# Kernel tuning notes

Measured on AMD Instinct MI355X. Metric: run time of the kernel, lower is better.

Reference implementation:

```python
import jax, jax.numpy as jnp
import numpy as np

N_NODES = 50000
N_EDGES = 400000
V = 3        # view_num
D = 128      # per-view input width (nfeat / view_num)
H = 128      # nhid


def setup_inputs() -> dict:
    key = jax.random.key(0)
    k_h, k_src, k_dst, k_w1, k_w2 = jax.random.split(key, 5)
    h = jax.random.normal(k_h, (N_NODES, V * D), dtype=jnp.float32)
    src = jax.random.randint(k_src, (N_EDGES,), 0, N_NODES, dtype=jnp.int32)
    dst = jax.random.randint(k_dst, (N_EDGES,), 0, N_NODES, dtype=jnp.int32)
    s1 = 1.0 / np.sqrt(D)
    s2 = 1.0 / np.sqrt(H)
    W1 = jax.random.uniform(k_w1, (V, D, H), dtype=jnp.float32, minval=-s1, maxval=s1)
    b1 = jnp.zeros((V, H), dtype=jnp.float32)
    W2 = jax.random.uniform(k_w2, (H, H), dtype=jnp.float32, minval=-s2, maxval=s2)
    b2 = jnp.zeros((H,), dtype=jnp.float32)
    return {"h": h, "src": src, "dst": dst, "W1": W1, "b1": b1, "W2": W2, "b2": b2}


def _agg(x, src, dst, n_nodes):
    # DGL GraphConv(norm='none') aggregation: out[d] = sum_{(s->d) in E} x[s]
    return jax.ops.segment_sum(x[src], dst, num_segments=n_nodes)


def reference(h, src, dst, W1, b1, W2, b2):
    n = h.shape[0]
    x = h.reshape(n, V, D)  # split into views along feature dim
    # layer 1 (per-view GraphConv + relu):  relu( A @ (x_v W1_v) + b1_v )
    xw = jnp.einsum('nvd,vdh->nvh', x, W1)
    y = jax.nn.relu(_agg(xw, src, dst, n) + b1)
    # dropout p=0 / eval mode -> identity
    # layer 2 (shared GraphConv + relu)
    yw = jnp.einsum('nvh,hk->nvk', y, W2)
    z = jax.nn.relu(_agg(yw, src, dst, n) + b2)
    # agg_type=0 -> plain concat of views
    return z.reshape(n, V * H)
```

## Files before the change

### kernel.cpp

```cpp
#include <hip/hip_runtime.h>

constexpr int NN = 50000;
constexpr int NE = 400000;
constexpr int NV = 3;
constexpr int DF = 128;
constexpr int F  = 384;
constexpr int TR = 32;
constexpr int NB = (NN + 255) / 256;
constexpr int SP = 136;

typedef short  bf16x8 __attribute__((ext_vector_type(8)));
typedef float  f32x4  __attribute__((ext_vector_type(4)));


__device__ __forceinline__ ushort f2bf(float f) {
  unsigned u = __float_as_uint(f);
  u = (u + 0x7fffu + ((u >> 16) & 1u)) >> 16;
  return (ushort)u;
}


__device__ __forceinline__ void wprep_one(const float* __restrict__ W,
                                          ushort* __restrict__ pk, int idx) {
  int j = idx & 7, lane = (idx >> 3) & 63, cb = (idx >> 9) & 7, kb = (idx >> 12) & 3;
  int vs = idx >> 14;
  int v = vs >> 1, s = vs & 1;
  int d = kb * 32 + (lane >> 4) * 8 + j;
  int c = cb * 16 + (lane & 15);
  float w = W[((size_t)v * DF + d) * DF + c];
  ushort hi = f2bf(w);
  ushort outv = hi;
  if (s) outv = f2bf(w - __uint_as_float((unsigned)hi << 16));
  pk[idx] = outv;
}

constexpr int WB1 = (NV * 2 * 16384) / 256;
constexpr int WB2 = (2 * 16384) / 256;

__global__ void k_prep0(const float* __restrict__ W1, const float* __restrict__ W2,
                        ushort* __restrict__ w1pk, ushort* __restrict__ w2pk,
                        int* __restrict__ deg) {
  int b = blockIdx.x, t = threadIdx.x;
  if (b < WB1) {
    wprep_one(W1, w1pk, b * 256 + t);
  } else if (b < WB1 + WB2) {
    wprep_one(W2, w2pk, (b - WB1) * 256 + t);
  } else {
    int i = (b - WB1 - WB2) * 256 + t;
    if (i < NN) deg[i] = 0;
  }
}


__global__ void k_cvtcnt(const float* __restrict__ in, ushort* __restrict__ outb,
                         const int* __restrict__ dst, int* __restrict__ deg) {
  int b = blockIdx.x, t = threadIdx.x;
  if (b < 2048) {
    const int n4 = NN * F / 4;
    const float4* in4 = (const float4*)in;
    for (int k = b * 256 + t; k < n4; k += 2048 * 256) {
      float4 x = in4[k];
      ushort4 u;
      u.x = f2bf(x.x); u.y = f2bf(x.y); u.z = f2bf(x.z); u.w = f2bf(x.w);
      *(ushort4*)(outb + (size_t)k * 4) = u;
    }
  } else {
    for (int e = (b - 2048) * 256 + t; e < NE; e += 1024 * 256)
      atomicAdd(&deg[dst[e]], 1);
  }
}


__global__ void k_blocksum(const int* __restrict__ deg, int* __restrict__ bsum) {
  __shared__ int s[4];
  int i = blockIdx.x * 256 + threadIdx.x;
  int v = (i < NN) ? deg[i] : 0;
  for (int o = 32; o > 0; o >>= 1) v += __shfl_down(v, o);
  if ((threadIdx.x & 63) == 0) s[threadIdx.x >> 6] = v;
  __syncthreads();
  if (threadIdx.x == 0) bsum[blockIdx.x] = s[0] + s[1] + s[2] + s[3];
}

__global__ void k_scanpar(int* __restrict__ bsum, int* __restrict__ offs_n) {
  __shared__ int s[256];
  int t = threadIdx.x;
  int v = (t < NB) ? bsum[t] : 0;
  s[t] = v;
  __syncthreads();
  for (int o = 1; o < 256; o <<= 1) {
    int add = (t >= o) ? s[t - o] : 0;
    __syncthreads();
    s[t] += add;
    __syncthreads();
  }
  if (t < NB) bsum[t] = s[t] - v;
  if (t == NB - 1) *offs_n = s[t];
}

__global__ void k_offsets(const int* __restrict__ deg, const int* __restrict__ bsum,
                          int* __restrict__ offs) {
  __shared__ int s[256];
  int t = threadIdx.x;
  int i = blockIdx.x * 256 + t;
  int v = (i < NN) ? deg[i] : 0;
  s[t] = v;
  __syncthreads();
  for (int o = 1; o < 256; o <<= 1) {
    int add = (t >= o) ? s[t - o] : 0;
    __syncthreads();
    s[t] += add;
    __syncthreads();
  }
  if (i < NN) offs[i] = bsum[blockIdx.x] + s[t] - v;
}

__global__ void k_scatter(const int* __restrict__ src, const int* __restrict__ dst,
                          const int* __restrict__ offs, int* __restrict__ deg,
                          int* __restrict__ csr) {
  int i = blockIdx.x * blockDim.x + threadIdx.x;
  int stride = gridDim.x * blockDim.x;
  for (int e = i; e < NE; e += stride) {
    int d = dst[e];
    int pos = offs[d] + atomicSub(&deg[d], 1) - 1;
    csr[pos] = src[e];
  }
}


template <bool OUT_BF16>
__global__ __launch_bounds__(256, 4)
void k_layer(const ushort* __restrict__ feat,
             const int* __restrict__ offs, const int* __restrict__ csr,
             const ushort* __restrict__ Wpk, int vmul,
             const float* __restrict__ ball, int bstride,
             void* __restrict__ outp) {
  __shared__ ushort sThi[TR][SP];
  __shared__ ushort sTlo[TR][SP];
  const int t = threadIdx.x;
  const int v = blockIdx.y;
  const float* __restrict__ bias = ball + (size_t)v * bstride;

  const int wave = t >> 6, lane = t & 63;
  const int lane15 = lane & 15, lgrp = lane >> 4;
  const int row0 = blockIdx.x * TR;
  const int vcol = v * DF + lane * 2;
  const int lane2 = lane * 2;

  const int base = row0 + wave * 8;

  int ow = 0;
  {
    int ri = base + lane;
    if (lane <= 8) {
      if (ri > NN) ri = NN;
      ow = offs[ri];
    }
  }
  int so[9];
#pragma unroll
  for (int k = 0; k < 9; ++k) so[k] = __builtin_amdgcn_readlane(ow, k);

  float ax[8], ay[8];
#pragma unroll
  for (int r = 0; r < 8; ++r) { ax[r] = 0.f; ay[r] = 0.f; }

  const int eb = so[0], ee = so[8];
  for (int chunk = eb; chunk < ee; chunk += 64) {
    int ce = chunk + lane; if (ce > ee - 1) ce = ee - 1;
    int idx = csr[ce];
    int cend = chunk + 64 < ee ? chunk + 64 : ee;
#pragma unroll
    for (int r = 0; r < 8; ++r) {
      int js = so[r] > chunk ? so[r] : chunk;
      int je = so[r + 1] < cend ? so[r + 1] : cend;
      int j  = js - chunk;
      int jn = je - chunk;
      for (; j + 4 <= jn; j += 4) {
        int s0 = __builtin_amdgcn_readlane(idx, j);
        int s1 = __builtin_amdgcn_readlane(idx, j + 1);
        int s2 = __builtin_amdgcn_readlane(idx, j + 2);
        int s3 = __builtin_amdgcn_readlane(idx, j + 3);
        unsigned u0 = *(const unsigned*)(feat + (size_t)s0 * F + vcol);
        unsigned u1 = *(const unsigned*)(feat + (size_t)s1 * F + vcol);
        unsigned u2 = *(const unsigned*)(feat + (size_t)s2 * F + vcol);
        unsigned u3 = *(const unsigned*)(feat + (size_t)s3 * F + vcol);
        ax[r] += __uint_as_float(u0 << 16); ay[r] += __uint_as_float(u0 & 0xffff0000u);
        ax[r] += __uint_as_float(u1 << 16); ay[r] += __uint_as_float(u1 & 0xffff0000u);
        ax[r] += __uint_as_float(u2 << 16); ay[r] += __uint_as_float(u2 & 0xffff0000u);
        ax[r] += __uint_as_float(u3 << 16); ay[r] += __uint_as_float(u3 & 0xffff0000u);
      }
      for (; j < jn; ++j) {
        int s0 = __builtin_amdgcn_readlane(idx, j);
        unsigned u0 = *(const unsigned*)(feat + (size_t)s0 * F + vcol);
        ax[r] += __uint_as_float(u0 << 16); ay[r] += __uint_as_float(u0 & 0xffff0000u);
      }
    }
  }

#pragma unroll
  for (int r = 0; r < 8; ++r) {
    ushort hx = f2bf(ax[r]);
    ushort lx = f2bf(ax[r] - __uint_as_float((unsigned)hx << 16));
    ushort hy = f2bf(ay[r]);
    ushort ly = f2bf(ay[r] - __uint_as_float((unsigned)hy << 16));
    *(unsigned*)&sThi[wave * 8 + r][lane2] = (unsigned)hx | ((unsigned)hy << 16);
    *(unsigned*)&sTlo[wave * 8 + r][lane2] = (unsigned)lx | ((unsigned)ly << 16);
  }
  __syncthreads();

  const ushort* pkbase = Wpk + (size_t)(v * vmul) * (2 * 4 * 8 * 512);
  const float bv0 = bias[wave * 32 + lane15];
  const float bv1 = bias[wave * 32 + 16 + lane15];
  f32x4 acc00 = {bv0, bv0, bv0, bv0};
  f32x4 acc01 = {bv1, bv1, bv1, bv1};
  f32x4 acc10 = {bv0, bv0, bv0, bv0};
  f32x4 acc11 = {bv1, bv1, bv1, bv1};

#pragma unroll
  for (int kb = 0; kb < 4; ++kb) {
    const int acol = kb * 32 + lgrp * 8;
    bf16x8 ah0 = *(const bf16x8*)&sThi[lane15][acol];
    bf16x8 ah1 = *(const bf16x8*)&sThi[16 + lane15][acol];
    bf16x8 al0 = *(const bf16x8*)&sTlo[lane15][acol];
    bf16x8 al1 = *(const bf16x8*)&sTlo[16 + lane15][acol];
    bf16x8 bh0 = *(const bf16x8*)(pkbase + ((size_t)((0 * 4 + kb) * 8 + wave * 2 + 0)) * 512 + lane * 8);
    bf16x8 bh1 = *(const bf16x8*)(pkbase + ((size_t)((0 * 4 + kb) * 8 + wave * 2 + 1)) * 512 + lane * 8);
    bf16x8 bl0 = *(const bf16x8*)(pkbase + ((size_t)((1 * 4 + kb) * 8 + wave * 2 + 0)) * 512 + lane * 8);
    bf16x8 bl1 = *(const bf16x8*)(pkbase + ((size_t)((1 * 4 + kb) * 8 + wave * 2 + 1)) * 512 + lane * 8);
    acc00 = __builtin_amdgcn_mfma_f32_16x16x32_bf16(ah0, bh0, acc00, 0, 0, 0);
    acc00 = __builtin_amdgcn_mfma_f32_16x16x32_bf16(al0, bh0, acc00, 0, 0, 0);
    acc00 = __builtin_amdgcn_mfma_f32_16x16x32_bf16(ah0, bl0, acc00, 0, 0, 0);
    acc01 = __builtin_amdgcn_mfma_f32_16x16x32_bf16(ah0, bh1, acc01, 0, 0, 0);
    acc01 = __builtin_amdgcn_mfma_f32_16x16x32_bf16(al0, bh1, acc01, 0, 0, 0);
    acc01 = __builtin_amdgcn_mfma_f32_16x16x32_bf16(ah0, bl1, acc01, 0, 0, 0);
    acc10 = __builtin_amdgcn_mfma_f32_16x16x32_bf16(ah1, bh0, acc10, 0, 0, 0);
    acc10 = __builtin_amdgcn_mfma_f32_16x16x32_bf16(al1, bh0, acc10, 0, 0, 0);
    acc10 = __builtin_amdgcn_mfma_f32_16x16x32_bf16(ah1, bl0, acc10, 0, 0, 0);
    acc11 = __builtin_amdgcn_mfma_f32_16x16x32_bf16(ah1, bh1, acc11, 0, 0, 0);
    acc11 = __builtin_amdgcn_mfma_f32_16x16x32_bf16(al1, bh1, acc11, 0, 0, 0);
    acc11 = __builtin_amdgcn_mfma_f32_16x16x32_bf16(ah1, bl1, acc11, 0, 0, 0);
  }

  const int colbase = v * DF + wave * 32 + lane15;
#pragma unroll
  for (int rb = 0; rb < 2; ++rb) {
    f32x4 a0 = rb ? acc10 : acc00;
    f32x4 a1 = rb ? acc11 : acc01;
#pragma unroll
    for (int k = 0; k < 4; ++k) {
      int row = row0 + rb * 16 + lgrp * 4 + k;
      if (row < NN) {
        float x0 = a0[k] > 0.f ? a0[k] : 0.f;
        float x1 = a1[k] > 0.f ? a1[k] : 0.f;
        if (OUT_BF16) {
          ushort* ob = (ushort*)outp;
          ob[(size_t)row * F + colbase]      = f2bf(x0);
          ob[(size_t)row * F + colbase + 16] = f2bf(x1);
        } else {
          float* of = (float*)outp;
          of[(size_t)row * F + colbase]      = x0;
          of[(size_t)row * F + colbase + 16] = x1;
        }
      }
    }
  }
}


static inline size_t align_up(size_t x, size_t a) { return (x + a - 1) & ~(a - 1); }

extern "C" void kernel_launch(void* const* d_in, const int* in_sizes, int n_in,
                              void* d_out, int out_size, void* d_ws, size_t ws_size,
                              hipStream_t stream) {
  const float* h   = (const float*)d_in[0];
  const int*   src = (const int*)d_in[1];
  const int*   dst = (const int*)d_in[2];
  const float* W1  = (const float*)d_in[3];
  const float* b1  = (const float*)d_in[4];
  const float* W2  = (const float*)d_in[5];
  const float* b2  = (const float*)d_in[6];
  float* out = (float*)d_out;

  char* ws = (char*)d_ws;
  size_t o = 0;
  int* deg  = (int*)(ws + o); o = align_up(o + (size_t)NN * 4, 1024);
  int* offs = (int*)(ws + o); o = align_up(o + (size_t)(NN + 1) * 4, 1024);
  int* bsum = (int*)(ws + o); o = align_up(o + 1024, 1024);
  int* csr  = (int*)(ws + o); o = align_up(o + (size_t)NE * 4, 1024);
  ushort* hb   = (ushort*)(ws + o); o = align_up(o + (size_t)NN * F * 2, 1024);
  ushort* ybuf = (ushort*)(ws + o); o = align_up(o + (size_t)NN * F * 2, 1024);
  ushort* w1pk = (ushort*)(ws + o); o = align_up(o + (size_t)NV * 2 * 16384 * 2, 1024);
  ushort* w2pk = (ushort*)(ws + o); o = align_up(o + (size_t)1 * 2 * 16384 * 2, 1024);
  (void)ws_size; (void)n_in; (void)in_sizes; (void)out_size;

  k_prep0<<<WB1 + WB2 + NB, 256, 0, stream>>>(W1, W2, w1pk, w2pk, deg);
  k_cvtcnt<<<3072, 256, 0, stream>>>(h, hb, dst, deg);
  k_blocksum<<<NB, 256, 0, stream>>>(deg, bsum);
  k_scanpar<<<1, 256, 0, stream>>>(bsum, offs + NN);
  k_offsets<<<NB, 256, 0, stream>>>(deg, bsum, offs);
  k_scatter<<<1024, 256, 0, stream>>>(src, dst, offs, deg, csr);

  dim3 grid((NN + TR - 1) / TR, NV);
  k_layer<true ><<<grid, 256, 0, stream>>>(hb,   offs, csr, w1pk, 1, b1, DF, ybuf);
  k_layer<false><<<grid, 256, 0, stream>>>(ybuf, offs, csr, w2pk, 0, b2, 0,  out);
}
```

Baseline: 196.1 us.

## Stage neighbor feature gathers through LDS with double-buffered async loads

The edge-gather loop now issues global_load_lds to copy each neighbor's feature dword straight into a per-wave LDS staging buffer, in batches of 16 edges with two buffers. A batch is accumulated from LDS while the next batch's loads are in flight, using explicit vmcnt waits. This aims to keep more gathers outstanding and hide gather latency, at the cost of extra LDS (32 KB more per block) and lower occupancy (launch bounds cut from 4 to 3 blocks). The hand-written waitcnt logic is fragile if the compiler emits other vector memory ops in the loop.

```diff
diff --git a/kernel.cpp b/kernel.cpp
--- a/kernel.cpp
+++ b/kernel.cpp
@@ -17,6 +17,12 @@
   unsigned u = __float_as_uint(f);
   u = (u + 0x7fffu + ((u >> 16) & 1u)) >> 16;
   return (ushort)u;
+}
+
+__device__ __forceinline__ void gload_lds4(const ushort* g, unsigned* ldsbase) {
+  __builtin_amdgcn_global_load_lds(
+      (const __attribute__((address_space(1))) void*)g,
+      (__attribute__((address_space(3))) void*)ldsbase, 4, 0, 0);
 }
 
 
@@ -128,7 +134,7 @@
 
 
 template <bool OUT_BF16>
-__global__ __launch_bounds__(256, 4)
+__global__ __launch_bounds__(256, 3)
 void k_layer(const ushort* __restrict__ feat,
              const int* __restrict__ offs, const int* __restrict__ csr,
              const ushort* __restrict__ Wpk, int vmul,
@@ -136,6 +142,7 @@
              void* __restrict__ outp) {
   __shared__ ushort sThi[TR][SP];
   __shared__ ushort sTlo[TR][SP];
+  __shared__ unsigned sStage[4][2][16][64];
   const int t = threadIdx.x;
   const int v = blockIdx.y;
   const float* __restrict__ bias = ball + (size_t)v * bstride;
@@ -165,36 +172,53 @@
   for (int r = 0; r < 8; ++r) { ax[r] = 0.f; ay[r] = 0.f; }
 
   const int eb = so[0], ee = so[8];
+
   for (int chunk = eb; chunk < ee; chunk += 64) {
     int ce = chunk + lane; if (ce > ee - 1) ce = ee - 1;
     int idx = csr[ce];
-    int cend = chunk + 64 < ee ? chunk + 64 : ee;
-#pragma unroll
-    for (int r = 0; r < 8; ++r) {
-      int js = so[r] > chunk ? so[r] : chunk;
-      int je = so[r + 1] < cend ? so[r + 1] : cend;
-      int j  = js - chunk;
-      int jn = je - chunk;
-      for (; j + 4 <= jn; j += 4) {
-        int s0 = __builtin_amdgcn_readlane(idx, j);
-        int s1 = __builtin_amdgcn_readlane(idx, j + 1);
-        int s2 = __builtin_amdgcn_readlane(idx, j + 2);
-        int s3 = __builtin_amdgcn_readlane(idx, j + 3);
-        unsigned u0 = *(const unsigned*)(feat + (size_t)s0 * F + vcol);
-        unsigned u1 = *(const unsigned*)(feat + (size_t)s1 * F + vcol);
-        unsigned u2 = *(const unsigned*)(feat + (size_t)s2 * F + vcol);
-        unsigned u3 = *(const unsigned*)(feat + (size_t)s3 * F + vcol);
-        ax[r] += __uint_as_float(u0 << 16); ay[r] += __uint_as_float(u0 & 0xffff0000u);
-        ax[r] += __uint_as_float(u1 << 16); ay[r] += __uint_as_float(u1 & 0xffff0000u);
-        ax[r] += __uint_as_float(u2 << 16); ay[r] += __uint_as_float(u2 & 0xffff0000u);
-        ax[r] += __uint_as_float(u3 << 16); ay[r] += __uint_as_float(u3 & 0xffff0000u);
-      }
-      for (; j < jn; ++j) {
-        int s0 = __builtin_amdgcn_readlane(idx, j);
-        unsigned u0 = *(const unsigned*)(feat + (size_t)s0 * F + vcol);
-        ax[r] += __uint_as_float(u0 << 16); ay[r] += __uint_as_float(u0 & 0xffff0000u);
-      }
-    }
+    int nb = ee - chunk; if (nb > 64) nb = 64;
+    int nbat = (nb + 15) >> 4;
+
+    auto accum = [&](int bb) {
+      int w0 = chunk + bb * 16;
+      int w1 = chunk + ((bb + 1) * 16 < nb ? (bb + 1) * 16 : nb);
+#pragma unroll
+      for (int r = 0; r < 8; ++r) {
+        int js = so[r] > w0 ? so[r] : w0;
+        int je = so[r + 1] < w1 ? so[r + 1] : w1;
+        for (int j = js; j < je; ++j) {
+          unsigned u = sStage[wave][bb & 1][j - w0][lane];
+          ax[r] += __uint_as_float(u << 16);
+          ay[r] += __uint_as_float(u & 0xffff0000u);
+        }
+      }
+    };
+
+    {
+      int e1 = nb < 16 ? nb : 16;
+      for (int e = 0; e < e1; ++e) {
+        int s = __builtin_amdgcn_readlane(idx, e);
+        gload_lds4(feat + (size_t)s * F + vcol, &sStage[wave][0][e][0]);
+      }
+    }
+    for (int b = 1; b < nbat; ++b) {
+      int e0 = b * 16;
+      int e1 = (b + 1) * 16 < nb ? (b + 1) * 16 : nb;
+      for (int e = e0; e < e1; ++e) {
+        int s = __builtin_amdgcn_readlane(idx, e);
+        gload_lds4(feat + (size_t)s * F + vcol, &sStage[wave][b & 1][e - e0][0]);
+      }
+      if (e1 - e0 == 16) {
+        asm volatile("s_waitcnt vmcnt(16)" ::: "memory");
+      } else {
+        asm volatile("s_waitcnt vmcnt(0)" ::: "memory");
+      }
+      __builtin_amdgcn_sched_barrier(0);
+      accum(b - 1);
+    }
+    asm volatile("s_waitcnt vmcnt(0)" ::: "memory");
+    __builtin_amdgcn_sched_barrier(0);
+    accum(nbat - 1);
   }
 
 #pragma unroll
```

After: 230.0 us. 17.3% more time.
